# Kernel optimization log

Hardware: AMD Instinct MI355X
Metric: run time of the kernel (lower is better)

Reference implementation:

```python
import jax, jax.numpy as jnp
import numpy as np

N_NODES = 100000
N_EDGES = 1600000


def setup_inputs() -> dict:
    key = jax.random.key(0)
    ks = jax.random.split(key, 12)
    s = lambda d: 1.0 / np.sqrt(d)
    inp = {
        "x": jax.random.normal(ks[0], (N_NODES, 64), dtype=jnp.float32),
        "edge_index": jax.random.randint(ks[1], (2, N_EDGES), 0, N_NODES, dtype=jnp.int64),
        "W_embed": jax.random.normal(ks[2], (64, 128), dtype=jnp.float32) * s(64),
        "eps1": jnp.zeros((), jnp.float32),
        "w1a": jax.random.normal(ks[3], (128, 128), dtype=jnp.float32) * s(128),
        "b1a": jnp.zeros((128,), jnp.float32),
        "w1b": jax.random.normal(ks[4], (128, 128), dtype=jnp.float32) * s(128),
        "b1b": jnp.zeros((128,), jnp.float32),
        "eps2": jnp.zeros((), jnp.float32),
        "w2a": jax.random.normal(ks[5], (128, 256), dtype=jnp.float32) * s(128),
        "b2a": jnp.zeros((256,), jnp.float32),
        "w2b": jax.random.normal(ks[6], (256, 128), dtype=jnp.float32) * s(256),
        "b2b": jnp.zeros((128,), jnp.float32),
        "eps3": jnp.zeros((), jnp.float32),
        "w3a": jax.random.normal(ks[7], (128, 256), dtype=jnp.float32) * s(128),
        "b3a": jnp.zeros((256,), jnp.float32),
        "w3b": jax.random.normal(ks[8], (256, 128), dtype=jnp.float32) * s(256),
        "b3b": jnp.zeros((128,), jnp.float32),
    }
    return inp


def _aggregate(h, src, dst, n):
    # GINConv sum aggregation: out[i] = sum_{(j,i) in E} h[j]
    return jax.ops.segment_sum(h[src], dst, num_segments=n)


def reference(x, edge_index, W_embed, eps1, w1a, b1a, w1b, b1b,
              eps2, w2a, b2a, w2b, b2b, eps3, w3a, b3a, w3b, b3b):
    src, dst = edge_index[0], edge_index[1]
    n = x.shape[0]
    # node_attr_encoder: linear embedding (dropout p=0 -> identity)
    h = x @ W_embed  # [N, dim]
    # conv1: nn((1+eps)*h + sum_neighbors), nn = Lin->ReLU->Lin
    z = (1.0 + eps1) * h + _aggregate(h, src, dst, n)
    h = jax.nn.relu(z @ w1a + b1a) @ w1b + b1b
    # conv2/conv3: nn = Lin->ReLU->Lin->ReLU
    z = (1.0 + eps2) * h + _aggregate(h, src, dst, n)
    h = jax.nn.relu(jax.nn.relu(z @ w2a + b2a) @ w2b + b2b)
    z = (1.0 + eps3) * h + _aggregate(h, src, dst, n)
    h = jax.nn.relu(jax.nn.relu(z @ w3a + b3a) @ w3b + b3b)
    return h
```

## Files before the change

### kernel.cpp

```cpp
#include <hip/hip_runtime.h>
#include <hip/hip_bf16.h>
#include <stdint.h>


typedef __attribute__((ext_vector_type(8))) short short8;
typedef __attribute__((ext_vector_type(16))) float float16v;
typedef __attribute__((ext_vector_type(4))) unsigned int uint4v;

#define BKT 512
#define NBMAX 256

#define MFMA32 __builtin_amdgcn_mfma_f32_32x32x16_bf16

union U4S8 { uint4v u; short8 s; };

__device__ __forceinline__ float b2f_lo(unsigned int u) {
    return __uint_as_float(u << 16);
}
__device__ __forceinline__ float b2f_hi(unsigned int u) {
    return __uint_as_float(u & 0xffff0000u);
}
__device__ __forceinline__ unsigned short f2b(float f) {
    unsigned int u = __float_as_uint(f);
    return (unsigned short)((u + 0x7fffu + ((u >> 16) & 1u)) >> 16);
}
__device__ __forceinline__ unsigned cvtpk_bf16(float a, float b) {
    unsigned r;
    asm("v_cvt_pk_bf16_f32 %0, %1, %2" : "=v"(r) : "v"(a), "v"(b));
    return r;
}
__device__ __forceinline__ void perm32swap(unsigned& a, unsigned& b) {
    asm("v_permlane32_swap_b32 %0, %1" : "+v"(a), "+v"(b));
}

__global__ void detect_i64_kernel(const unsigned int* ei, int* flag) {
    if (threadIdx.x == 0) {
        int is64 = 1;
        for (int e = 0; e < 64; ++e)
            if (ei[2 * e + 1] != 0u) { is64 = 0; break; }
        *flag = is64;
    }
}

__device__ __forceinline__ int edge_at(const int* ei32, int is64, long long pos) {
    if (is64) return (int)(((const long long*)ei32)[pos]);
    return ei32[pos];
}

__global__ __launch_bounds__(256) void part_hist_kernel(
        const int* __restrict__ ei, const int* __restrict__ flag,
        int* __restrict__ bh, int E, int NB, int PB) {
    __shared__ int h[NBMAX];
    const int g = blockIdx.x, tid = threadIdx.x;
    const int is64 = *flag;
    for (int i = tid; i < NB; i += 256) h[i] = 0;
    __syncthreads();
    const int e0 = g * PB, e1 = min(e0 + PB, E);
    for (int e = e0 + tid; e < e1; e += 256) {
        int d = edge_at(ei, is64, (long long)E + e);
        atomicAdd(&h[d >> 9], 1);
    }
    __syncthreads();
    for (int i = tid; i < NB; i += 256) bh[i * gridDim.x + g] = h[i];
}

__global__ __launch_bounds__(1024) void scan1_kernel(
        const int* __restrict__ in, int* __restrict__ out,
        int* __restrict__ partial, int n) {
    __shared__ int sm[1024];
    const int t = threadIdx.x;
    const int i = blockIdx.x * 1024 + t;
    int v = (i < n) ? in[i] : 0;
    sm[t] = v;
    __syncthreads();
#pragma unroll
    for (int off = 1; off < 1024; off <<= 1) {
        int x = (t >= off) ? sm[t - off] : 0;
        __syncthreads();
        sm[t] += x;
        __syncthreads();
    }
    if (i < n) out[i] = sm[t] - v;
    if (t == 1023) partial[blockIdx.x] = sm[1023];
}

__global__ __launch_bounds__(256) void scan2_kernel(
        int* __restrict__ partial, int* __restrict__ blockoff, int g1) {
    __shared__ int sm[256];
    const int t = threadIdx.x;
    int v = (t < g1) ? partial[t] : 0;
    sm[t] = v;
    __syncthreads();
#pragma unroll
    for (int off = 1; off < 256; off <<= 1) {
        int x = (t >= off) ? sm[t - off] : 0;
        __syncthreads();
        sm[t] += x;
        __syncthreads();
    }
    blockoff[t] = sm[t] - v;
}

__global__ __launch_bounds__(1024) void scan3g_kernel(
        int* __restrict__ a, const int* __restrict__ blockoff, int n) {
    int i = blockIdx.x * 1024 + threadIdx.x;
    if (i < n) a[i] += blockoff[blockIdx.x];
}

__global__ __launch_bounds__(256) void part_scatter_kernel(
        const int* __restrict__ ei, const int* __restrict__ flag,
        const int* __restrict__ bhs, unsigned int* __restrict__ staged,
        int E, int NB, int PB) {
    __shared__ int cur[NBMAX];
    const int g = blockIdx.x, tid = threadIdx.x;
    const int is64 = *flag;
    for (int i = tid; i < NB; i += 256) cur[i] = bhs[i * gridDim.x + g];
    __syncthreads();
    const int e0 = g * PB, e1 = min(e0 + PB, E);
    for (int e = e0 + tid; e < e1; e += 256) {
        int d = edge_at(ei, is64, (long long)E + e);
        int s = edge_at(ei, is64, (long long)e);
        int b = d >> 9;
        int p = atomicAdd(&cur[b], 1);
        staged[p] = ((unsigned int)(d & (BKT - 1)) << 17) | (unsigned int)s;
    }
}

__global__ __launch_bounds__(256) void csr_local_kernel(
        const unsigned int* __restrict__ staged, const int* __restrict__ bhs,
        int* __restrict__ offs, int* __restrict__ csr, int N, int E, int NB, int G2) {
    __shared__ int hist[BKT];
    __shared__ int cur[BKT];
    const int b = blockIdx.x;
    const int tid = threadIdx.x;
    const int start = bhs[b * G2];
    const int end = (b + 1 < NB) ? bhs[(b + 1) * G2] : E;
    const int node0 = b * BKT;
    for (int i = tid; i < BKT; i += 256) hist[i] = 0;
    __syncthreads();
    for (int i = start + tid; i < end; i += 256)
        atomicAdd(&hist[staged[i] >> 17], 1);
    __syncthreads();
    const int i0 = tid * 2, i1 = i0 + 1;
    for (int off = 1; off < BKT; off <<= 1) {
        int v0 = (i0 >= off) ? hist[i0 - off] : 0;
        int v1 = (i1 >= off) ? hist[i1 - off] : 0;
        __syncthreads();
        hist[i0] += v0;
        hist[i1] += v1;
        __syncthreads();
    }
    for (int i = tid; i < BKT; i += 256) {
        int node = node0 + i;
        if (node < N) {
            int e0 = start + ((i == 0) ? 0 : hist[i - 1]);
            offs[node] = e0;
            cur[i] = e0;
        }
    }
    if (b == NB - 1 && tid == 0) offs[N] = E;
    __syncthreads();
    for (int i = start + tid; i < end; i += 256) {
        unsigned int v = staged[i];
        int dl = v >> 17;
        int src = (int)(v & 0x1ffff);
        int p = atomicAdd(&cur[dl], 1);
        csr[p] = src;
    }
}

struct PW { const float* W; unsigned short* o; int K; int KOUT; };
struct PWAll { PW d[7]; int cum[8]; };

__global__ __launch_bounds__(256) void packall_kernel(PWAll P) {
    int id = blockIdx.x * blockDim.x + threadIdx.x;
    if (id >= P.cum[7]) return;
    int w = 0;
#pragma unroll
    for (int k = 1; k < 7; ++k) w += (id >= P.cum[k]);
    const int local = id - P.cum[w];
    const float* W = P.d[w].W;
    unsigned short* out = P.d[w].o;
    const int K = P.d[w].K, KOUT = P.d[w].KOUT;
    const int KS = K / 16;
    const int l = local & 63;
    const int s = (local >> 6) % KS;
    const int T = local / (KS * 64);
    const int kbase = s * 16 + ((l >> 5) << 3);
    const int n = T * 32 + (l & 31);
#pragma unroll
    for (int j = 0; j < 8; ++j)
        out[(long long)local * 8 + j] = f2b(W[(long long)(kbase + j) * KOUT + n]);
}

__global__ __launch_bounds__(256) void mm_embed(
        const float* __restrict__ X, const unsigned short* __restrict__ Wp,
        unsigned short* __restrict__ out, int Mreal) {
    constexpr int KS = 4;
    const int tid = threadIdx.x;
    const int w = tid >> 6;
    const int l = tid & 63;
    const int lm = l & 31;
    const int lk = l >> 5;
    const int wr = w & 1, wc = w >> 1;
    const long long R0 = (long long)blockIdx.x * 128 + wr * 64;
    const int T0 = (wc * 64) >> 5;

    const long long r0 = (R0 + lm < Mreal) ? (R0 + lm) : (Mreal - 1);
    const long long r1 = (R0 + 32 + lm < Mreal) ? (R0 + 32 + lm) : (Mreal - 1);
    const float* xr0 = X + r0 * 64 + lk * 8;
    const float* xr1 = X + r1 * 64 + lk * 8;
    const unsigned short* bb0 = Wp + ((long long)T0 * KS * 64 + l) * 8;
    const unsigned short* bb1 = Wp + ((long long)(T0 + 1) * KS * 64 + l) * 8;

    float16v acc00 = {}, acc01 = {}, acc10 = {}, acc11 = {};
#pragma unroll
    for (int s = 0; s < KS; ++s) {
        float4 f0a = *(const float4*)(xr0 + s * 16);
        float4 f0b = *(const float4*)(xr0 + s * 16 + 4);
        float4 f1a = *(const float4*)(xr1 + s * 16);
        float4 f1b = *(const float4*)(xr1 + s * 16 + 4);
        short8 a0, a1;
        a0[0] = (short)f2b(f0a.x); a0[1] = (short)f2b(f0a.y);
        a0[2] = (short)f2b(f0a.z); a0[3] = (short)f2b(f0a.w);
        a0[4] = (short)f2b(f0b.x); a0[5] = (short)f2b(f0b.y);
        a0[6] = (short)f2b(f0b.z); a0[7] = (short)f2b(f0b.w);
        a1[0] = (short)f2b(f1a.x); a1[1] = (short)f2b(f1a.y);
        a1[2] = (short)f2b(f1a.z); a1[3] = (short)f2b(f1a.w);
        a1[4] = (short)f2b(f1b.x); a1[5] = (short)f2b(f1b.y);
        a1[6] = (short)f2b(f1b.z); a1[7] = (short)f2b(f1b.w);
        short8 b0 = *(const short8*)(bb0 + (long long)s * 64 * 8);
        short8 b1 = *(const short8*)(bb1 + (long long)s * 64 * 8);
        acc00 = MFMA32(a0, b0, acc00, 0, 0, 0);
        acc01 = MFMA32(a0, b1, acc01, 0, 0, 0);
        acc10 = MFMA32(a1, b0, acc10, 0, 0, 0);
        acc11 = MFMA32(a1, b1, acc11, 0, 0, 0);
    }
    auto st = [&](float16v acc, long long rb, int col) {
#pragma unroll
        for (int r = 0; r < 16; ++r) {
            long long row = rb + (r & 3) + 8 * (r >> 2);
            out[row * 128 + col] = f2b(acc[r]);
        }
    };
    const long long rbase = R0 + 4 * lk;
    st(acc00, rbase,      wc * 64 + lm);
    st(acc01, rbase,      wc * 64 + 32 + lm);
    st(acc10, rbase + 32, wc * 64 + lm);
    st(acc11, rbase + 32, wc * 64 + 32 + lm);
}

__global__ __launch_bounds__(256) void aggz_kernel(
        const unsigned short* __restrict__ H, const int* __restrict__ offs,
        const int* __restrict__ csr, const float* __restrict__ eps,
        unsigned short* __restrict__ Z, int n) {
    const int node = blockIdx.x * 16 + (threadIdx.x >> 4);
    const int c8 = (threadIdx.x & 15) << 3;
    if (node >= n) return;
    const int beg = offs[node];
    const int end = offs[node + 1];
    float a0 = 0.f, a1 = 0.f, a2 = 0.f, a3 = 0.f;
    float a4 = 0.f, a5 = 0.f, a6 = 0.f, a7 = 0.f;
    int i = beg;
    for (; i + 3 < end; i += 4) {
        const int j0 = csr[i], j1 = csr[i + 1], j2 = csr[i + 2], j3 = csr[i + 3];
        const uint4 u0 = *(const uint4*)(H + ((long long)j0 << 7) + c8);
        const uint4 u1 = *(const uint4*)(H + ((long long)j1 << 7) + c8);
        const uint4 u2 = *(const uint4*)(H + ((long long)j2 << 7) + c8);
        const uint4 u3 = *(const uint4*)(H + ((long long)j3 << 7) + c8);
        a0 += (b2f_lo(u0.x) + b2f_lo(u1.x)) + (b2f_lo(u2.x) + b2f_lo(u3.x));
        a1 += (b2f_hi(u0.x) + b2f_hi(u1.x)) + (b2f_hi(u2.x) + b2f_hi(u3.x));
        a2 += (b2f_lo(u0.y) + b2f_lo(u1.y)) + (b2f_lo(u2.y) + b2f_lo(u3.y));
        a3 += (b2f_hi(u0.y) + b2f_hi(u1.y)) + (b2f_hi(u2.y) + b2f_hi(u3.y));
        a4 += (b2f_lo(u0.z) + b2f_lo(u1.z)) + (b2f_lo(u2.z) + b2f_lo(u3.z));
        a5 += (b2f_hi(u0.z) + b2f_hi(u1.z)) + (b2f_hi(u2.z) + b2f_hi(u3.z));
        a6 += (b2f_lo(u0.w) + b2f_lo(u1.w)) + (b2f_lo(u2.w) + b2f_lo(u3.w));
        a7 += (b2f_hi(u0.w) + b2f_hi(u1.w)) + (b2f_hi(u2.w) + b2f_hi(u3.w));
    }
    for (; i < end; ++i) {
        const uint4 u0 = *(const uint4*)(H + ((long long)csr[i] << 7) + c8);
        a0 += b2f_lo(u0.x); a1 += b2f_hi(u0.x);
        a2 += b2f_lo(u0.y); a3 += b2f_hi(u0.y);
        a4 += b2f_lo(u0.z); a5 += b2f_hi(u0.z);
        a6 += b2f_lo(u0.w); a7 += b2f_hi(u0.w);
    }
    const uint4 uh = *(const uint4*)(H + ((long long)node << 7) + c8);
    const float e = 1.0f + eps[0];
    a0 = fmaf(e, b2f_lo(uh.x), a0); a1 = fmaf(e, b2f_hi(uh.x), a1);
    a2 = fmaf(e, b2f_lo(uh.y), a2); a3 = fmaf(e, b2f_hi(uh.y), a3);
    a4 = fmaf(e, b2f_lo(uh.z), a4); a5 = fmaf(e, b2f_hi(uh.z), a5);
    a6 = fmaf(e, b2f_lo(uh.w), a6); a7 = fmaf(e, b2f_hi(uh.w), a7);
    uint4 o;
    o.x = ((unsigned int)f2b(a1) << 16) | (unsigned int)f2b(a0);
    o.y = ((unsigned int)f2b(a3) << 16) | (unsigned int)f2b(a2);
    o.z = ((unsigned int)f2b(a5) << 16) | (unsigned int)f2b(a4);
    o.w = ((unsigned int)f2b(a7) << 16) | (unsigned int)f2b(a6);
    *(uint4*)(Z + ((long long)node << 7) + c8) = o;
}


#define CVT_TO_PA2(ACC, P0, P1) do {                                   \
        unsigned X1 = cvtpk_bf16((ACC)[0], (ACC)[1]);                  \
        unsigned Y1 = cvtpk_bf16((ACC)[4], (ACC)[5]);                  \
        unsigned X2 = cvtpk_bf16((ACC)[2], (ACC)[3]);                  \
        unsigned Y2 = cvtpk_bf16((ACC)[6], (ACC)[7]);                  \
        perm32swap(X1, Y1); perm32swap(X2, Y2);                        \
        U4S8 u0; u0.u[0] = X1; u0.u[1] = X2; u0.u[2] = Y1; u0.u[3] = Y2; \
        (P0) = u0.s;                                                   \
        unsigned X3 = cvtpk_bf16((ACC)[8], (ACC)[9]);                  \
        unsigned Y3 = cvtpk_bf16((ACC)[12], (ACC)[13]);                \
        unsigned X4 = cvtpk_bf16((ACC)[10], (ACC)[11]);                \
        unsigned Y4 = cvtpk_bf16((ACC)[14], (ACC)[15]);                \
        perm32swap(X3, Y3); perm32swap(X4, Y4);                        \
        U4S8 u1; u1.u[0] = X3; u1.u[1] = X4; u1.u[2] = Y3; u1.u[3] = Y4; \
        (P1) = u1.s;                                                   \
    } while (0)

template<int KMID, bool RELU2, bool OUTF32>
__global__ __launch_bounds__(512, 2) void fused_mlp3(
        const unsigned short* __restrict__ Zin,
        const unsigned short* __restrict__ Wap, const float* __restrict__ ba,
        const unsigned short* __restrict__ Wbp, const float* __restrict__ bb,
        void* __restrict__ outp, int Mreal, int nstrips) {
    constexpr int NF = KMID / 32;
    constexpr int NCH = KMID / 16;
    constexpr int WAS = 128 * KMID;
    __shared__ unsigned short wlds[KMID * 256];
    __shared__ float blds[KMID + 128];
    const int tid = threadIdx.x;

    {
        const uint4* sa = (const uint4*)Wap;
        const uint4* sb = (const uint4*)Wbp;
        uint4* da = (uint4*)wlds;
        uint4* db = (uint4*)(wlds + WAS);
#pragma unroll
        for (int i = tid; i < KMID * 16; i += 512) { da[i] = sa[i]; db[i] = sb[i]; }
        for (int i = tid; i < KMID; i += 512) blds[i] = ba[i];
        if (tid < 128) blds[KMID + tid] = bb[tid];
    }
    __syncthreads();

    const int wid = tid >> 6;
    const int l = tid & 63;
    const int lo = l & 31;
    const int hi = l >> 5;
    const int stride = gridDim.x * 8;
    int strip = blockIdx.x * 8 + wid;
    if (strip >= nstrips) return;

    auto zload = [&](int s_, short8* zz) {
        long long zr = (long long)s_ * 32 + lo;
        if (zr >= Mreal) zr = Mreal - 1;
        const unsigned short* zrow = Zin + zr * 128 + hi * 8;
#pragma unroll
        for (int s = 0; s < 8; ++s) zz[s] = *(const short8*)(zrow + s * 16);
    };

    short8 zc[8];
    zload(strip, zc);

    while (strip < nstrips) {
        const int nxt = strip + stride;
        float16v acc2[4] = {};
        short8 zn[8];

#pragma unroll
        for (int fp = 0; fp < NF / 2; ++fp) {
            if (fp == NF / 2 - 1) {
                if (nxt < nstrips) zload(nxt, zn);
            }
            const int f0 = 2 * fp, f1 = f0 + 1;
            float16v accA, accB;
#pragma unroll
            for (int q = 0; q < 4; ++q) {
                const float4 tA = *(const float4*)(blds + f0 * 32 + q * 8 + hi * 4);
                const float4 tB = *(const float4*)(blds + f1 * 32 + q * 8 + hi * 4);
                accA[4 * q + 0] = tA.x; accA[4 * q + 1] = tA.y;
                accA[4 * q + 2] = tA.z; accA[4 * q + 3] = tA.w;
                accB[4 * q + 0] = tB.x; accB[4 * q + 1] = tB.y;
                accB[4 * q + 2] = tB.z; accB[4 * q + 3] = tB.w;
            }
            const unsigned short* wa0 = wlds + ((long long)(f0 * 8) * 64 + l) * 8;
            const unsigned short* wa1 = wlds + ((long long)(f1 * 8) * 64 + l) * 8;
#pragma unroll
            for (int s = 0; s < 8; ++s) {
                short8 a0 = *(const short8*)(wa0 + s * 64 * 8);
                short8 a1 = *(const short8*)(wa1 + s * 64 * 8);
                accA = MFMA32(a0, zc[s], accA, 0, 0, 0);
                accB = MFMA32(a1, zc[s], accB, 0, 0, 0);
            }
#pragma unroll
            for (int r = 0; r < 16; ++r) {
                accA[r] = fmaxf(accA[r], 0.f);
                accB[r] = fmaxf(accB[r], 0.f);
            }
            short8 pa0, pa1, pa2, pa3;
            CVT_TO_PA2(accA, pa0, pa1);
            CVT_TO_PA2(accB, pa2, pa3);
            const unsigned short* wb = wlds + WAS + ((long long)(fp * 4) * 64 + l) * 8;
#pragma unroll
            for (int g = 0; g < 4; ++g) {
                const unsigned short* wbg = wb + (long long)g * NCH * 64 * 8;
                short8 b0 = *(const short8*)(wbg);
                short8 b1 = *(const short8*)(wbg + 64 * 8);
                short8 b2 = *(const short8*)(wbg + 2 * 64 * 8);
                short8 b3 = *(const short8*)(wbg + 3 * 64 * 8);
                acc2[g] = MFMA32(pa0, b0, acc2[g], 0, 0, 0);
                acc2[g] = MFMA32(pa1, b1, acc2[g], 0, 0, 0);
                acc2[g] = MFMA32(pa2, b2, acc2[g], 0, 0, 0);
                acc2[g] = MFMA32(pa3, b3, acc2[g], 0, 0, 0);
            }
        }

#pragma unroll
        for (int g = 0; g < 4; ++g) {
            const int col = g * 32 + lo;
            const float bv = blds[KMID + col];
#pragma unroll
            for (int r = 0; r < 16; ++r) {
                float v = acc2[g][r] + bv;
                if (RELU2) v = fmaxf(v, 0.f);
                const long long node = (long long)strip * 32 + (r & 3) + 8 * (r >> 2) + 4 * hi;
                if (node < Mreal) {
                    if (OUTF32) ((float*)outp)[node * 128 + col] = v;
                    else ((unsigned short*)outp)[node * 128 + col] = f2b(v);
                }
            }
        }

        strip = nxt;
        if (strip < nstrips) {
#pragma unroll
            for (int s = 0; s < 8; ++s) zc[s] = zn[s];
        }
    }
}

extern "C" void kernel_launch(void* const* d_in, const int* in_sizes, int n_in,
                              void* d_out, int out_size, void* d_ws, size_t ws_size,
                              hipStream_t stream) {
    const float* x    = (const float*)d_in[0];
    const int*   ei   = (const int*)d_in[1];
    const float* Wemb = (const float*)d_in[2];
    const float* eps1 = (const float*)d_in[3];
    const float* w1a  = (const float*)d_in[4];
    const float* b1a  = (const float*)d_in[5];
    const float* w1b  = (const float*)d_in[6];
    const float* b1b  = (const float*)d_in[7];
    const float* eps2 = (const float*)d_in[8];
    const float* w2a  = (const float*)d_in[9];
    const float* b2a  = (const float*)d_in[10];
    const float* w2b  = (const float*)d_in[11];
    const float* b2b  = (const float*)d_in[12];
    const float* eps3 = (const float*)d_in[13];
    const float* w3a  = (const float*)d_in[14];
    const float* b3a  = (const float*)d_in[15];
    const float* w3b  = (const float*)d_in[16];
    const float* b3b  = (const float*)d_in[17];

    const int N = in_sizes[0] / 64;
    const int E = in_sizes[1] / 2;
    const int Mpad = ((N + 127) / 128) * 128;
    const int NB = (N + BKT - 1) / BKT;
    const int G2 = 1024;
    const int PB = (E + G2 - 1) / G2;
    const int BH = NB * G2;

    char* ws = (char*)d_ws;
    size_t off = 0;
    auto alloc = [&](size_t bytes) -> void* {
        void* p = ws + off;
        off = (off + bytes + 255) & ~(size_t)255;
        return p;
    };
    unsigned short* Ha  = (unsigned short*)alloc((size_t)Mpad * 128 * 2);
    unsigned short* Hb2 = (unsigned short*)alloc((size_t)Mpad * 128 * 2);
    unsigned short* Zb  = (unsigned short*)alloc((size_t)Mpad * 128 * 2);
    unsigned short* pWe = (unsigned short*)alloc((size_t)64 * 128 * 2);
    unsigned short* p1a = (unsigned short*)alloc((size_t)128 * 128 * 2);
    unsigned short* p1b = (unsigned short*)alloc((size_t)128 * 128 * 2);
    unsigned short* p2a = (unsigned short*)alloc((size_t)128 * 256 * 2);
    unsigned short* p2b = (unsigned short*)alloc((size_t)256 * 128 * 2);
    unsigned short* p3a = (unsigned short*)alloc((size_t)128 * 256 * 2);
    unsigned short* p3b = (unsigned short*)alloc((size_t)256 * 128 * 2);
    int* offs = (int*)alloc((size_t)(N + 1) * 4);
    int* csr  = (int*)alloc((size_t)E * 4);
    unsigned int* staged = (unsigned int*)alloc((size_t)E * 4);
    int* bh   = (int*)alloc((size_t)BH * 4);
    int* bhs  = (int*)alloc((size_t)BH * 4);
    int* part = (int*)alloc(1024);
    int* boff = (int*)alloc(1024);
    int* flag = (int*)alloc(256);

    detect_i64_kernel<<<1, 64, 0, stream>>>((const unsigned int*)ei, flag);
    part_hist_kernel<<<G2, 256, 0, stream>>>(ei, flag, bh, E, NB, PB);
    const int G1 = (BH + 1023) / 1024;
    scan1_kernel<<<G1, 1024, 0, stream>>>(bh, bhs, part, BH);
    scan2_kernel<<<1, 256, 0, stream>>>(part, boff, G1);
    scan3g_kernel<<<G1, 1024, 0, stream>>>(bhs, boff, BH);
    part_scatter_kernel<<<G2, 256, 0, stream>>>(ei, flag, bhs, staged, E, NB, PB);
    csr_local_kernel<<<NB, 256, 0, stream>>>(staged, bhs, offs, csr, N, E, NB, G2);

    {
        PWAll P;
        const PW descs[7] = {
            {Wemb, pWe, 64, 128}, {w1a, p1a, 128, 128}, {w1b, p1b, 128, 128},
            {w2a, p2a, 128, 256}, {w2b, p2b, 256, 128}, {w3a, p3a, 128, 256},
            {w3b, p3b, 256, 128}};
        int c = 0;
        for (int k = 0; k < 7; ++k) {
            P.d[k] = descs[k];
            P.cum[k] = c;
            c += (descs[k].KOUT / 32) * (descs[k].K / 16) * 64;
        }
        P.cum[7] = c;
        packall_kernel<<<(c + 255) / 256, 256, 0, stream>>>(P);
    }

    const int MMB = Mpad / 128;
    const int AGB = (N + 15) / 16;
    const int NSTRIP = (N + 31) / 32;
    const int MLPG = 256;

    mm_embed<<<MMB, 256, 0, stream>>>(x, pWe, Ha, N);

    aggz_kernel<<<AGB, 256, 0, stream>>>(Ha, offs, csr, eps1, Zb, N);
    fused_mlp3<128, false, false><<<MLPG, 512, 0, stream>>>(Zb, p1a, b1a, p1b, b1b, Hb2, N, NSTRIP);

    aggz_kernel<<<AGB, 256, 0, stream>>>(Hb2, offs, csr, eps2, Zb, N);
    fused_mlp3<256, true, false><<<MLPG, 512, 0, stream>>>(Zb, p2a, b2a, p2b, b2b, Ha, N, NSTRIP);

    aggz_kernel<<<AGB, 256, 0, stream>>>(Ha, offs, csr, eps3, Zb, N);
    fused_mlp3<256, true, true><<<MLPG, 512, 0, stream>>>(Zb, p3a, b3a, p3b, b3b, d_out, N, NSTRIP);
}
```

Measured before the change: 435.4 us.

## Add 12-wave fused MLP kernel reading Z from global; inline int64 detection

Adds fused_mlp5, a 768-thread MLP kernel where each wave handles its own 32-node strip. It reads Z rows straight from global memory instead of the register-prefetched pipeline of fused_mlp3. The new kernel replaces layers 1 and 3, while layer 2 keeps the old kernel. The separate int64 detection kernel is removed, and each block of the partition kernels now detects the index width itself. The aim is more waves for latency hiding and one fewer launch, at the cost of redundant detection reads and less explicit prefetching.

```diff
diff --git a/kernel.cpp b/kernel.cpp
--- a/kernel.cpp
+++ b/kernel.cpp
@@ -33,28 +33,28 @@
     asm("v_permlane32_swap_b32 %0, %1" : "+v"(a), "+v"(b));
 }
 
-__global__ void detect_i64_kernel(const unsigned int* ei, int* flag) {
-    if (threadIdx.x == 0) {
-        int is64 = 1;
-        for (int e = 0; e < 64; ++e)
-            if (ei[2 * e + 1] != 0u) { is64 = 0; break; }
-        *flag = is64;
-    }
-}
-
 __device__ __forceinline__ int edge_at(const int* ei32, int is64, long long pos) {
     if (is64) return (int)(((const long long*)ei32)[pos]);
     return ei32[pos];
 }
 
+__device__ __forceinline__ int detect_is64(const int* ei) {
+    const unsigned int* eu = (const unsigned int*)ei;
+    int is64 = 1;
+    for (int e = 0; e < 64; ++e)
+        if (eu[2 * e + 1] != 0u) { is64 = 0; break; }
+    return is64;
+}
+
 __global__ __launch_bounds__(256) void part_hist_kernel(
-        const int* __restrict__ ei, const int* __restrict__ flag,
-        int* __restrict__ bh, int E, int NB, int PB) {
+        const int* __restrict__ ei, int* __restrict__ bh, int E, int NB, int PB) {
     __shared__ int h[NBMAX];
+    __shared__ int is64sh;
     const int g = blockIdx.x, tid = threadIdx.x;
-    const int is64 = *flag;
     for (int i = tid; i < NB; i += 256) h[i] = 0;
-    __syncthreads();
+    if (tid == 0) is64sh = detect_is64(ei);
+    __syncthreads();
+    const int is64 = is64sh;
     const int e0 = g * PB, e1 = min(e0 + PB, E);
     for (int e = e0 + tid; e < e1; e += 256) {
         int d = edge_at(ei, is64, (long long)E + e);
@@ -108,14 +108,15 @@
 }
 
 __global__ __launch_bounds__(256) void part_scatter_kernel(
-        const int* __restrict__ ei, const int* __restrict__ flag,
-        const int* __restrict__ bhs, unsigned int* __restrict__ staged,
-        int E, int NB, int PB) {
+        const int* __restrict__ ei, const int* __restrict__ bhs,
+        unsigned int* __restrict__ staged, int E, int NB, int PB) {
     __shared__ int cur[NBMAX];
+    __shared__ int is64sh;
     const int g = blockIdx.x, tid = threadIdx.x;
-    const int is64 = *flag;
     for (int i = tid; i < NB; i += 256) cur[i] = bhs[i * gridDim.x + g];
-    __syncthreads();
+    if (tid == 0) is64sh = detect_is64(ei);
+    __syncthreads();
+    const int is64 = is64sh;
     const int e0 = g * PB, e1 = min(e0 + PB, E);
     for (int e = e0 + tid; e < e1; e += 256) {
         int d = edge_at(ei, is64, (long long)E + e);
@@ -298,7 +299,6 @@
     *(uint4*)(Z + ((long long)node << 7) + c8) = o;
 }
 
-
 #define CVT_TO_PA2(ACC, P0, P1) do {                                   \
         unsigned X1 = cvtpk_bf16((ACC)[0], (ACC)[1]);                  \
         unsigned Y1 = cvtpk_bf16((ACC)[4], (ACC)[5]);                  \
@@ -433,6 +433,105 @@
         if (strip < nstrips) {
 #pragma unroll
             for (int s = 0; s < 8; ++s) zc[s] = zn[s];
+        }
+    }
+}
+
+template<int KMID, bool RELU2, bool OUTF32>
+__global__ __launch_bounds__(768, 3) void fused_mlp5(
+        const unsigned short* __restrict__ Zin,
+        const unsigned short* __restrict__ Wap, const float* __restrict__ ba,
+        const unsigned short* __restrict__ Wbp, const float* __restrict__ bb,
+        void* __restrict__ outp, int Mreal, int nstrips) {
+    constexpr int NF = KMID / 32;
+    constexpr int NCH = KMID / 16;
+    constexpr int WAS = 128 * KMID;
+    __shared__ unsigned short wlds[KMID * 256];
+    __shared__ float blds[KMID + 128];
+    const int tid = threadIdx.x;
+
+    {
+        const uint4* sa = (const uint4*)Wap;
+        const uint4* sb = (const uint4*)Wbp;
+        uint4* da = (uint4*)wlds;
+        uint4* db = (uint4*)(wlds + WAS);
+        for (int i = tid; i < KMID * 16; i += 768) { da[i] = sa[i]; db[i] = sb[i]; }
+        for (int i = tid; i < KMID; i += 768) blds[i] = ba[i];
+        if (tid < 128) blds[KMID + tid] = bb[tid];
+    }
+    __syncthreads();
+
+    const int wid = tid >> 6;
+    const int l = tid & 63;
+    const int lo = l & 31;
+    const int hi = l >> 5;
+    const int stride = gridDim.x * 12;
+
+    for (int strip = blockIdx.x * 12 + wid; strip < nstrips; strip += stride) {
+        const long long node0 = (long long)strip * 32;
+        long long zr = node0 + lo;
+        if (zr >= Mreal) zr = Mreal - 1;
+        const unsigned short* zrow = Zin + zr * 128 + hi * 8;
+
+        float16v acc2[4] = {};
+
+#pragma unroll 1
+        for (int f = 0; f < NF; ++f) {
+            float16v accA;
+#pragma unroll
+            for (int q = 0; q < 4; ++q) {
+                const float4 tA = *(const float4*)(blds + f * 32 + q * 8 + hi * 4);
+                accA[4 * q + 0] = tA.x; accA[4 * q + 1] = tA.y;
+                accA[4 * q + 2] = tA.z; accA[4 * q + 3] = tA.w;
+            }
+            const unsigned short* wa = wlds + (f * 8 * 64 + l) * 8;
+            {
+                short8 z0 = *(const short8*)(zrow + 0 * 16);
+                short8 z1 = *(const short8*)(zrow + 1 * 16);
+                short8 z2 = *(const short8*)(zrow + 2 * 16);
+                short8 z3 = *(const short8*)(zrow + 3 * 16);
+                accA = MFMA32(*(const short8*)(wa + 0 * 64 * 8), z0, accA, 0, 0, 0);
+                accA = MFMA32(*(const short8*)(wa + 1 * 64 * 8), z1, accA, 0, 0, 0);
+                accA = MFMA32(*(const short8*)(wa + 2 * 64 * 8), z2, accA, 0, 0, 0);
+                accA = MFMA32(*(const short8*)(wa + 3 * 64 * 8), z3, accA, 0, 0, 0);
+            }
+            {
+                short8 z4 = *(const short8*)(zrow + 4 * 16);
+                short8 z5 = *(const short8*)(zrow + 5 * 16);
+                short8 z6 = *(const short8*)(zrow + 6 * 16);
+                short8 z7 = *(const short8*)(zrow + 7 * 16);
+                accA = MFMA32(*(const short8*)(wa + 4 * 64 * 8), z4, accA, 0, 0, 0);
+                accA = MFMA32(*(const short8*)(wa + 5 * 64 * 8), z5, accA, 0, 0, 0);
+                accA = MFMA32(*(const short8*)(wa + 6 * 64 * 8), z6, accA, 0, 0, 0);
+                accA = MFMA32(*(const short8*)(wa + 7 * 64 * 8), z7, accA, 0, 0, 0);
+            }
+#pragma unroll
+            for (int r = 0; r < 16; ++r) accA[r] = fmaxf(accA[r], 0.f);
+            short8 pa0, pa1;
+            CVT_TO_PA2(accA, pa0, pa1);
+            const unsigned short* wb = wlds + WAS + ((2 * f) * 64 + l) * 8;
+#pragma unroll
+            for (int g = 0; g < 4; ++g) {
+                const unsigned short* wbg = wb + g * NCH * 64 * 8;
+                acc2[g] = MFMA32(pa0, *(const short8*)(wbg), acc2[g], 0, 0, 0);
+                acc2[g] = MFMA32(pa1, *(const short8*)(wbg + 64 * 8), acc2[g], 0, 0, 0);
+            }
+        }
+
+#pragma unroll
+        for (int g = 0; g < 4; ++g) {
+            const int col = g * 32 + lo;
+            const float bv = blds[KMID + col];
+#pragma unroll
+            for (int r = 0; r < 16; ++r) {
+                float v = acc2[g][r] + bv;
+                if (RELU2) v = fmaxf(v, 0.f);
+                const long long node = node0 + (r & 3) + 8 * (r >> 2) + 4 * hi;
+                if (node < Mreal) {
+                    if (OUTF32) ((float*)outp)[node * 128 + col] = v;
+                    else ((unsigned short*)outp)[node * 128 + col] = f2b(v);
+                }
+            }
         }
     }
 }
@@ -491,15 +590,13 @@
     int* bhs  = (int*)alloc((size_t)BH * 4);
     int* part = (int*)alloc(1024);
     int* boff = (int*)alloc(1024);
-    int* flag = (int*)alloc(256);
-
-    detect_i64_kernel<<<1, 64, 0, stream>>>((const unsigned int*)ei, flag);
-    part_hist_kernel<<<G2, 256, 0, stream>>>(ei, flag, bh, E, NB, PB);
+
+    part_hist_kernel<<<G2, 256, 0, stream>>>(ei, bh, E, NB, PB);
     const int G1 = (BH + 1023) / 1024;
     scan1_kernel<<<G1, 1024, 0, stream>>>(bh, bhs, part, BH);
     scan2_kernel<<<1, 256, 0, stream>>>(part, boff, G1);
     scan3g_kernel<<<G1, 1024, 0, stream>>>(bhs, boff, BH);
-    part_scatter_kernel<<<G2, 256, 0, stream>>>(ei, flag, bhs, staged, E, NB, PB);
+    part_scatter_kernel<<<G2, 256, 0, stream>>>(ei, bhs, staged, E, NB, PB);
     csr_local_kernel<<<NB, 256, 0, stream>>>(staged, bhs, offs, csr, N, E, NB, G2);
 
     {
@@ -526,11 +623,11 @@
     mm_embed<<<MMB, 256, 0, stream>>>(x, pWe, Ha, N);
 
     aggz_kernel<<<AGB, 256, 0, stream>>>(Ha, offs, csr, eps1, Zb, N);
-    fused_mlp3<128, false, false><<<MLPG, 512, 0, stream>>>(Zb, p1a, b1a, p1b, b1b, Hb2, N, NSTRIP);
+    fused_mlp5<128, false, false><<<MLPG, 768, 0, stream>>>(Zb, p1a, b1a, p1b, b1b, Hb2, N, NSTRIP);
 
     aggz_kernel<<<AGB, 256, 0, stream>>>(Hb2, offs, csr, eps2, Zb, N);
     fused_mlp3<256, true, false><<<MLPG, 512, 0, stream>>>(Zb, p2a, b2a, p2b, b2b, Ha, N, NSTRIP);
 
     aggz_kernel<<<AGB, 256, 0, stream>>>(Ha, offs, csr, eps3, Zb, N);
-    fused_mlp3<256, true, true><<<MLPG, 512, 0, stream>>>(Zb, p3a, b3a, p3b, b3b, d_out, N, NSTRIP);
-}
+    fused_mlp5<256, true, true><<<MLPG, 768, 0, stream>>>(Zb, p3a, b3a, p3b, b3b, d_out, N, NSTRIP);
+}
```

Result: no change. 436.0 us (+0.1%).

## Fuse neighbor aggregation into MLP kernel and fold int64 detection into partition kernels

Applied to the files above, without the earlier changes.

Each wave now gathers neighbor rows for its own 32-node strip, writes the aggregated Z rows to a global scratch buffer, and reads them back for the MFMA MLP. This removes three aggregation launches and lets gather latency overlap with MLP work in other waves. The standalone int64-detect kernel is also dropped; each partition block does the check itself. In exchange, the aggregation now runs on only 256 blocks of 512 threads with launch bounds tuned for the MLP, so it loses the wide parallelism of the old gather kernel, and the next-strip Z prefetch is gone.

```diff
diff --git a/kernel.cpp b/kernel.cpp
--- a/kernel.cpp
+++ b/kernel.cpp
@@ -33,28 +33,28 @@
     asm("v_permlane32_swap_b32 %0, %1" : "+v"(a), "+v"(b));
 }
 
-__global__ void detect_i64_kernel(const unsigned int* ei, int* flag) {
-    if (threadIdx.x == 0) {
-        int is64 = 1;
-        for (int e = 0; e < 64; ++e)
-            if (ei[2 * e + 1] != 0u) { is64 = 0; break; }
-        *flag = is64;
-    }
-}
-
 __device__ __forceinline__ int edge_at(const int* ei32, int is64, long long pos) {
     if (is64) return (int)(((const long long*)ei32)[pos]);
     return ei32[pos];
 }
 
+__device__ __forceinline__ int detect_is64(const int* ei) {
+    const unsigned int* eu = (const unsigned int*)ei;
+    int is64 = 1;
+    for (int e = 0; e < 64; ++e)
+        if (eu[2 * e + 1] != 0u) { is64 = 0; break; }
+    return is64;
+}
+
 __global__ __launch_bounds__(256) void part_hist_kernel(
-        const int* __restrict__ ei, const int* __restrict__ flag,
-        int* __restrict__ bh, int E, int NB, int PB) {
+        const int* __restrict__ ei, int* __restrict__ bh, int E, int NB, int PB) {
     __shared__ int h[NBMAX];
+    __shared__ int is64sh;
     const int g = blockIdx.x, tid = threadIdx.x;
-    const int is64 = *flag;
     for (int i = tid; i < NB; i += 256) h[i] = 0;
-    __syncthreads();
+    if (tid == 0) is64sh = detect_is64(ei);
+    __syncthreads();
+    const int is64 = is64sh;
     const int e0 = g * PB, e1 = min(e0 + PB, E);
     for (int e = e0 + tid; e < e1; e += 256) {
         int d = edge_at(ei, is64, (long long)E + e);
@@ -108,14 +108,15 @@
 }
 
 __global__ __launch_bounds__(256) void part_scatter_kernel(
-        const int* __restrict__ ei, const int* __restrict__ flag,
-        const int* __restrict__ bhs, unsigned int* __restrict__ staged,
-        int E, int NB, int PB) {
+        const int* __restrict__ ei, const int* __restrict__ bhs,
+        unsigned int* __restrict__ staged, int E, int NB, int PB) {
     __shared__ int cur[NBMAX];
+    __shared__ int is64sh;
     const int g = blockIdx.x, tid = threadIdx.x;
-    const int is64 = *flag;
     for (int i = tid; i < NB; i += 256) cur[i] = bhs[i * gridDim.x + g];
-    __syncthreads();
+    if (tid == 0) is64sh = detect_is64(ei);
+    __syncthreads();
+    const int is64 = is64sh;
     const int e0 = g * PB, e1 = min(e0 + PB, E);
     for (int e = e0 + tid; e < e1; e += 256) {
         int d = edge_at(ei, is64, (long long)E + e);
@@ -250,55 +251,6 @@
     st(acc11, rbase + 32, wc * 64 + 32 + lm);
 }
 
-__global__ __launch_bounds__(256) void aggz_kernel(
-        const unsigned short* __restrict__ H, const int* __restrict__ offs,
-        const int* __restrict__ csr, const float* __restrict__ eps,
-        unsigned short* __restrict__ Z, int n) {
-    const int node = blockIdx.x * 16 + (threadIdx.x >> 4);
-    const int c8 = (threadIdx.x & 15) << 3;
-    if (node >= n) return;
-    const int beg = offs[node];
-    const int end = offs[node + 1];
-    float a0 = 0.f, a1 = 0.f, a2 = 0.f, a3 = 0.f;
-    float a4 = 0.f, a5 = 0.f, a6 = 0.f, a7 = 0.f;
-    int i = beg;
-    for (; i + 3 < end; i += 4) {
-        const int j0 = csr[i], j1 = csr[i + 1], j2 = csr[i + 2], j3 = csr[i + 3];
-        const uint4 u0 = *(const uint4*)(H + ((long long)j0 << 7) + c8);
-        const uint4 u1 = *(const uint4*)(H + ((long long)j1 << 7) + c8);
-        const uint4 u2 = *(const uint4*)(H + ((long long)j2 << 7) + c8);
-        const uint4 u3 = *(const uint4*)(H + ((long long)j3 << 7) + c8);
-        a0 += (b2f_lo(u0.x) + b2f_lo(u1.x)) + (b2f_lo(u2.x) + b2f_lo(u3.x));
-        a1 += (b2f_hi(u0.x) + b2f_hi(u1.x)) + (b2f_hi(u2.x) + b2f_hi(u3.x));
-        a2 += (b2f_lo(u0.y) + b2f_lo(u1.y)) + (b2f_lo(u2.y) + b2f_lo(u3.y));
-        a3 += (b2f_hi(u0.y) + b2f_hi(u1.y)) + (b2f_hi(u2.y) + b2f_hi(u3.y));
-        a4 += (b2f_lo(u0.z) + b2f_lo(u1.z)) + (b2f_lo(u2.z) + b2f_lo(u3.z));
-        a5 += (b2f_hi(u0.z) + b2f_hi(u1.z)) + (b2f_hi(u2.z) + b2f_hi(u3.z));
-        a6 += (b2f_lo(u0.w) + b2f_lo(u1.w)) + (b2f_lo(u2.w) + b2f_lo(u3.w));
-        a7 += (b2f_hi(u0.w) + b2f_hi(u1.w)) + (b2f_hi(u2.w) + b2f_hi(u3.w));
-    }
-    for (; i < end; ++i) {
-        const uint4 u0 = *(const uint4*)(H + ((long long)csr[i] << 7) + c8);
-        a0 += b2f_lo(u0.x); a1 += b2f_hi(u0.x);
-        a2 += b2f_lo(u0.y); a3 += b2f_hi(u0.y);
-        a4 += b2f_lo(u0.z); a5 += b2f_hi(u0.z);
-        a6 += b2f_lo(u0.w); a7 += b2f_hi(u0.w);
-    }
-    const uint4 uh = *(const uint4*)(H + ((long long)node << 7) + c8);
-    const float e = 1.0f + eps[0];
-    a0 = fmaf(e, b2f_lo(uh.x), a0); a1 = fmaf(e, b2f_hi(uh.x), a1);
-    a2 = fmaf(e, b2f_lo(uh.y), a2); a3 = fmaf(e, b2f_hi(uh.y), a3);
-    a4 = fmaf(e, b2f_lo(uh.z), a4); a5 = fmaf(e, b2f_hi(uh.z), a5);
-    a6 = fmaf(e, b2f_lo(uh.w), a6); a7 = fmaf(e, b2f_hi(uh.w), a7);
-    uint4 o;
-    o.x = ((unsigned int)f2b(a1) << 16) | (unsigned int)f2b(a0);
-    o.y = ((unsigned int)f2b(a3) << 16) | (unsigned int)f2b(a2);
-    o.z = ((unsigned int)f2b(a5) << 16) | (unsigned int)f2b(a4);
-    o.w = ((unsigned int)f2b(a7) << 16) | (unsigned int)f2b(a6);
-    *(uint4*)(Z + ((long long)node << 7) + c8) = o;
-}
-
-
 #define CVT_TO_PA2(ACC, P0, P1) do {                                   \
         unsigned X1 = cvtpk_bf16((ACC)[0], (ACC)[1]);                  \
         unsigned Y1 = cvtpk_bf16((ACC)[4], (ACC)[5]);                  \
@@ -317,8 +269,11 @@
     } while (0)
 
 template<int KMID, bool RELU2, bool OUTF32>
-__global__ __launch_bounds__(512, 2) void fused_mlp3(
-        const unsigned short* __restrict__ Zin,
+__global__ __launch_bounds__(512, 2) void fused_aggmlp(
+        const unsigned short* __restrict__ H,
+        const int* __restrict__ offs, const int* __restrict__ csr,
+        const float* __restrict__ epsp,
+        unsigned short* __restrict__ Zb,
         const unsigned short* __restrict__ Wap, const float* __restrict__ ba,
         const unsigned short* __restrict__ Wbp, const float* __restrict__ bb,
         void* __restrict__ outp, int Mreal, int nstrips) {
@@ -345,31 +300,71 @@
     const int l = tid & 63;
     const int lo = l & 31;
     const int hi = l >> 5;
+    const int c8 = (l & 15) << 3;
+    const float e = 1.0f + epsp[0];
     const int stride = gridDim.x * 8;
-    int strip = blockIdx.x * 8 + wid;
-    if (strip >= nstrips) return;
-
-    auto zload = [&](int s_, short8* zz) {
-        long long zr = (long long)s_ * 32 + lo;
+
+    for (int strip = blockIdx.x * 8 + wid; strip < nstrips; strip += stride) {
+        const long long node0 = (long long)strip * 32;
+
+        const unsigned short* Hc = H + c8;
+#pragma unroll 1
+        for (int rnd = 0; rnd < 8; ++rnd) {
+            const int node = (int)node0 + rnd * 4 + (l >> 4);
+            if (node < Mreal) {
+                const int beg = offs[node];
+                const int end = offs[node + 1];
+                float a0 = 0.f, a1 = 0.f, a2 = 0.f, a3 = 0.f;
+                float a4 = 0.f, a5 = 0.f, a6 = 0.f, a7 = 0.f;
+                int i = beg;
+                for (; i + 3 < end; i += 4) {
+                    const int j0 = csr[i], j1 = csr[i + 1], j2 = csr[i + 2], j3 = csr[i + 3];
+                    const uint4 u0 = *(const uint4*)(Hc + ((long long)j0 << 7));
+                    const uint4 u1 = *(const uint4*)(Hc + ((long long)j1 << 7));
+                    const uint4 u2 = *(const uint4*)(Hc + ((long long)j2 << 7));
+                    const uint4 u3 = *(const uint4*)(Hc + ((long long)j3 << 7));
+                    a0 += (b2f_lo(u0.x) + b2f_lo(u1.x)) + (b2f_lo(u2.x) + b2f_lo(u3.x));
+                    a1 += (b2f_hi(u0.x) + b2f_hi(u1.x)) + (b2f_hi(u2.x) + b2f_hi(u3.x));
+                    a2 += (b2f_lo(u0.y) + b2f_lo(u1.y)) + (b2f_lo(u2.y) + b2f_lo(u3.y));
+                    a3 += (b2f_hi(u0.y) + b2f_hi(u1.y)) + (b2f_hi(u2.y) + b2f_hi(u3.y));
+                    a4 += (b2f_lo(u0.z) + b2f_lo(u1.z)) + (b2f_lo(u2.z) + b2f_lo(u3.z));
+                    a5 += (b2f_hi(u0.z) + b2f_hi(u1.z)) + (b2f_hi(u2.z) + b2f_hi(u3.z));
+                    a6 += (b2f_lo(u0.w) + b2f_lo(u1.w)) + (b2f_lo(u2.w) + b2f_lo(u3.w));
+                    a7 += (b2f_hi(u0.w) + b2f_hi(u1.w)) + (b2f_hi(u2.w) + b2f_hi(u3.w));
+                }
+                for (; i < end; ++i) {
+                    const uint4 u0 = *(const uint4*)(Hc + ((long long)csr[i] << 7));
+                    a0 += b2f_lo(u0.x); a1 += b2f_hi(u0.x);
+                    a2 += b2f_lo(u0.y); a3 += b2f_hi(u0.y);
+                    a4 += b2f_lo(u0.z); a5 += b2f_hi(u0.z);
+                    a6 += b2f_lo(u0.w); a7 += b2f_hi(u0.w);
+                }
+                const uint4 uh = *(const uint4*)(Hc + ((long long)node << 7));
+                a0 = fmaf(e, b2f_lo(uh.x), a0); a1 = fmaf(e, b2f_hi(uh.x), a1);
+                a2 = fmaf(e, b2f_lo(uh.y), a2); a3 = fmaf(e, b2f_hi(uh.y), a3);
+                a4 = fmaf(e, b2f_lo(uh.z), a4); a5 = fmaf(e, b2f_hi(uh.z), a5);
+                a6 = fmaf(e, b2f_lo(uh.w), a6); a7 = fmaf(e, b2f_hi(uh.w), a7);
+                uint4 o;
+                o.x = ((unsigned int)f2b(a1) << 16) | (unsigned int)f2b(a0);
+                o.y = ((unsigned int)f2b(a3) << 16) | (unsigned int)f2b(a2);
+                o.z = ((unsigned int)f2b(a5) << 16) | (unsigned int)f2b(a4);
+                o.w = ((unsigned int)f2b(a7) << 16) | (unsigned int)f2b(a6);
+                *(uint4*)(Zb + ((long long)node << 7) + c8) = o;
+            }
+        }
+        asm volatile("s_waitcnt vmcnt(0)" ::: "memory");
+
+        long long zr = node0 + lo;
         if (zr >= Mreal) zr = Mreal - 1;
-        const unsigned short* zrow = Zin + zr * 128 + hi * 8;
-#pragma unroll
-        for (int s = 0; s < 8; ++s) zz[s] = *(const short8*)(zrow + s * 16);
-    };
-
-    short8 zc[8];
-    zload(strip, zc);
-
-    while (strip < nstrips) {
-        const int nxt = strip + stride;
+        const unsigned short* zrow = Zb + zr * 128 + hi * 8;
+        short8 zc[8];
+#pragma unroll
+        for (int s = 0; s < 8; ++s) zc[s] = *(const short8*)(zrow + s * 16);
+
         float16v acc2[4] = {};
-        short8 zn[8];
 
 #pragma unroll
         for (int fp = 0; fp < NF / 2; ++fp) {
-            if (fp == NF / 2 - 1) {
-                if (nxt < nstrips) zload(nxt, zn);
-            }
             const int f0 = 2 * fp, f1 = f0 + 1;
             float16v accA, accB;
 #pragma unroll
@@ -421,18 +416,12 @@
             for (int r = 0; r < 16; ++r) {
                 float v = acc2[g][r] + bv;
                 if (RELU2) v = fmaxf(v, 0.f);
-                const long long node = (long long)strip * 32 + (r & 3) + 8 * (r >> 2) + 4 * hi;
+                const long long node = node0 + (r & 3) + 8 * (r >> 2) + 4 * hi;
                 if (node < Mreal) {
                     if (OUTF32) ((float*)outp)[node * 128 + col] = v;
                     else ((unsigned short*)outp)[node * 128 + col] = f2b(v);
                 }
             }
-        }
-
-        strip = nxt;
-        if (strip < nstrips) {
-#pragma unroll
-            for (int s = 0; s < 8; ++s) zc[s] = zn[s];
         }
     }
 }
@@ -491,15 +480,13 @@
     int* bhs  = (int*)alloc((size_t)BH * 4);
     int* part = (int*)alloc(1024);
     int* boff = (int*)alloc(1024);
-    int* flag = (int*)alloc(256);
-
-    detect_i64_kernel<<<1, 64, 0, stream>>>((const unsigned int*)ei, flag);
-    part_hist_kernel<<<G2, 256, 0, stream>>>(ei, flag, bh, E, NB, PB);
+
+    part_hist_kernel<<<G2, 256, 0, stream>>>(ei, bh, E, NB, PB);
     const int G1 = (BH + 1023) / 1024;
     scan1_kernel<<<G1, 1024, 0, stream>>>(bh, bhs, part, BH);
     scan2_kernel<<<1, 256, 0, stream>>>(part, boff, G1);
     scan3g_kernel<<<G1, 1024, 0, stream>>>(bhs, boff, BH);
-    part_scatter_kernel<<<G2, 256, 0, stream>>>(ei, flag, bhs, staged, E, NB, PB);
+    part_scatter_kernel<<<G2, 256, 0, stream>>>(ei, bhs, staged, E, NB, PB);
     csr_local_kernel<<<NB, 256, 0, stream>>>(staged, bhs, offs, csr, N, E, NB, G2);
 
     {
@@ -519,18 +506,17 @@
     }
 
     const int MMB = Mpad / 128;
-    const int AGB = (N + 15) / 16;
     const int NSTRIP = (N + 31) / 32;
     const int MLPG = 256;
 
     mm_embed<<<MMB, 256, 0, stream>>>(x, pWe, Ha, N);
 
-    aggz_kernel<<<AGB, 256, 0, stream>>>(Ha, offs, csr, eps1, Zb, N);
-    fused_mlp3<128, false, false><<<MLPG, 512, 0, stream>>>(Zb, p1a, b1a, p1b, b1b, Hb2, N, NSTRIP);
-
-    aggz_kernel<<<AGB, 256, 0, stream>>>(Hb2, offs, csr, eps2, Zb, N);
-    fused_mlp3<256, true, false><<<MLPG, 512, 0, stream>>>(Zb, p2a, b2a, p2b, b2b, Ha, N, NSTRIP);
-
-    aggz_kernel<<<AGB, 256, 0, stream>>>(Ha, offs, csr, eps3, Zb, N);
-    fused_mlp3<256, true, true><<<MLPG, 512, 0, stream>>>(Zb, p3a, b3a, p3b, b3b, d_out, N, NSTRIP);
-}
+    fused_aggmlp<128, false, false><<<MLPG, 512, 0, stream>>>(
+        Ha, offs, csr, eps1, Zb, p1a, b1a, p1b, b1b, Hb2, N, NSTRIP);
+
+    fused_aggmlp<256, true, false><<<MLPG, 512, 0, stream>>>(
+        Hb2, offs, csr, eps2, Zb, p2a, b2a, p2b, b2b, Ha, N, NSTRIP);
+
+    fused_aggmlp<256, true, true><<<MLPG, 512, 0, stream>>>(
+        Ha, offs, csr, eps3, Zb, p3a, b3a, p3b, b3b, d_out, N, NSTRIP);
+}
```

After: 584.5 us. +34.3%, slower.

## Use atomic work-stealing for MLP strips and fold i64 detection into partition kernels

Applied to the files above, without the earlier changes.

The fused MLP kernels now hand out 32-row strips through a global atomic counter per layer instead of a fixed grid stride, so waves that finish early pick up more work. The counters are zeroed inside the embedding kernel. The separate int64-detect launch is removed and each partition block now repeats the detection itself. The conv2 MLP grid also drops to 128 blocks. This trades one kernel launch and static imbalance for an atomic per strip per wave, redundant detection reads in every block, and a dependence on mm_embed running before the MLPs to reset the counters.

```diff
diff --git a/kernel.cpp b/kernel.cpp
--- a/kernel.cpp
+++ b/kernel.cpp
@@ -33,28 +33,28 @@
     asm("v_permlane32_swap_b32 %0, %1" : "+v"(a), "+v"(b));
 }
 
-__global__ void detect_i64_kernel(const unsigned int* ei, int* flag) {
-    if (threadIdx.x == 0) {
-        int is64 = 1;
-        for (int e = 0; e < 64; ++e)
-            if (ei[2 * e + 1] != 0u) { is64 = 0; break; }
-        *flag = is64;
-    }
-}
-
 __device__ __forceinline__ int edge_at(const int* ei32, int is64, long long pos) {
     if (is64) return (int)(((const long long*)ei32)[pos]);
     return ei32[pos];
 }
 
+__device__ __forceinline__ int detect_is64(const int* ei) {
+    const unsigned int* eu = (const unsigned int*)ei;
+    int is64 = 1;
+    for (int e = 0; e < 64; ++e)
+        if (eu[2 * e + 1] != 0u) { is64 = 0; break; }
+    return is64;
+}
+
 __global__ __launch_bounds__(256) void part_hist_kernel(
-        const int* __restrict__ ei, const int* __restrict__ flag,
-        int* __restrict__ bh, int E, int NB, int PB) {
+        const int* __restrict__ ei, int* __restrict__ bh, int E, int NB, int PB) {
     __shared__ int h[NBMAX];
+    __shared__ int is64sh;
     const int g = blockIdx.x, tid = threadIdx.x;
-    const int is64 = *flag;
     for (int i = tid; i < NB; i += 256) h[i] = 0;
-    __syncthreads();
+    if (tid == 0) is64sh = detect_is64(ei);
+    __syncthreads();
+    const int is64 = is64sh;
     const int e0 = g * PB, e1 = min(e0 + PB, E);
     for (int e = e0 + tid; e < e1; e += 256) {
         int d = edge_at(ei, is64, (long long)E + e);
@@ -108,14 +108,15 @@
 }
 
 __global__ __launch_bounds__(256) void part_scatter_kernel(
-        const int* __restrict__ ei, const int* __restrict__ flag,
-        const int* __restrict__ bhs, unsigned int* __restrict__ staged,
-        int E, int NB, int PB) {
+        const int* __restrict__ ei, const int* __restrict__ bhs,
+        unsigned int* __restrict__ staged, int E, int NB, int PB) {
     __shared__ int cur[NBMAX];
+    __shared__ int is64sh;
     const int g = blockIdx.x, tid = threadIdx.x;
-    const int is64 = *flag;
     for (int i = tid; i < NB; i += 256) cur[i] = bhs[i * gridDim.x + g];
-    __syncthreads();
+    if (tid == 0) is64sh = detect_is64(ei);
+    __syncthreads();
+    const int is64 = is64sh;
     const int e0 = g * PB, e1 = min(e0 + PB, E);
     for (int e = e0 + tid; e < e1; e += 256) {
         int d = edge_at(ei, is64, (long long)E + e);
@@ -195,9 +196,10 @@
 
 __global__ __launch_bounds__(256) void mm_embed(
         const float* __restrict__ X, const unsigned short* __restrict__ Wp,
-        unsigned short* __restrict__ out, int Mreal) {
+        unsigned short* __restrict__ out, int Mreal, int* __restrict__ ctrs) {
     constexpr int KS = 4;
     const int tid = threadIdx.x;
+    if (blockIdx.x == 0 && tid < 3) ctrs[tid] = 0;
     const int w = tid >> 6;
     const int l = tid & 63;
     const int lm = l & 31;
@@ -298,7 +300,6 @@
     *(uint4*)(Z + ((long long)node << 7) + c8) = o;
 }
 
-
 #define CVT_TO_PA2(ACC, P0, P1) do {                                   \
         unsigned X1 = cvtpk_bf16((ACC)[0], (ACC)[1]);                  \
         unsigned Y1 = cvtpk_bf16((ACC)[4], (ACC)[5]);                  \
@@ -317,11 +318,11 @@
     } while (0)
 
 template<int KMID, bool RELU2, bool OUTF32>
-__global__ __launch_bounds__(512, 2) void fused_mlp3(
+__global__ __launch_bounds__(512, 2) void fused_mlp6(
         const unsigned short* __restrict__ Zin,
         const unsigned short* __restrict__ Wap, const float* __restrict__ ba,
         const unsigned short* __restrict__ Wbp, const float* __restrict__ bb,
-        void* __restrict__ outp, int Mreal, int nstrips) {
+        void* __restrict__ outp, int Mreal, int nstrips, int* __restrict__ ctr) {
     constexpr int NF = KMID / 32;
     constexpr int NCH = KMID / 16;
     constexpr int WAS = 128 * KMID;
@@ -341,13 +342,15 @@
     }
     __syncthreads();
 
-    const int wid = tid >> 6;
     const int l = tid & 63;
     const int lo = l & 31;
     const int hi = l >> 5;
-    const int stride = gridDim.x * 8;
-    int strip = blockIdx.x * 8 + wid;
-    if (strip >= nstrips) return;
+
+    auto steal = [&]() -> int {
+        int s = 0;
+        if (l == 0) s = atomicAdd(ctr, 1);
+        return __shfl(s, 0);
+    };
 
     auto zload = [&](int s_, short8* zz) {
         long long zr = (long long)s_ * 32 + lo;
@@ -357,11 +360,13 @@
         for (int s = 0; s < 8; ++s) zz[s] = *(const short8*)(zrow + s * 16);
     };
 
+    int strip = steal();
+    if (strip >= nstrips) return;
     short8 zc[8];
     zload(strip, zc);
 
-    while (strip < nstrips) {
-        const int nxt = strip + stride;
+    while (true) {
+        const int nxt = steal();
         float16v acc2[4] = {};
         short8 zn[8];
 
@@ -429,11 +434,10 @@
             }
         }
 
+        if (nxt >= nstrips) break;
         strip = nxt;
-        if (strip < nstrips) {
-#pragma unroll
-            for (int s = 0; s < 8; ++s) zc[s] = zn[s];
-        }
+#pragma unroll
+        for (int s = 0; s < 8; ++s) zc[s] = zn[s];
     }
 }
 
@@ -491,15 +495,14 @@
     int* bhs  = (int*)alloc((size_t)BH * 4);
     int* part = (int*)alloc(1024);
     int* boff = (int*)alloc(1024);
-    int* flag = (int*)alloc(256);
-
-    detect_i64_kernel<<<1, 64, 0, stream>>>((const unsigned int*)ei, flag);
-    part_hist_kernel<<<G2, 256, 0, stream>>>(ei, flag, bh, E, NB, PB);
+    int* mctr = (int*)alloc(256);
+
+    part_hist_kernel<<<G2, 256, 0, stream>>>(ei, bh, E, NB, PB);
     const int G1 = (BH + 1023) / 1024;
     scan1_kernel<<<G1, 1024, 0, stream>>>(bh, bhs, part, BH);
     scan2_kernel<<<1, 256, 0, stream>>>(part, boff, G1);
     scan3g_kernel<<<G1, 1024, 0, stream>>>(bhs, boff, BH);
-    part_scatter_kernel<<<G2, 256, 0, stream>>>(ei, flag, bhs, staged, E, NB, PB);
+    part_scatter_kernel<<<G2, 256, 0, stream>>>(ei, bhs, staged, E, NB, PB);
     csr_local_kernel<<<NB, 256, 0, stream>>>(staged, bhs, offs, csr, N, E, NB, G2);
 
     {
@@ -521,16 +524,18 @@
     const int MMB = Mpad / 128;
     const int AGB = (N + 15) / 16;
     const int NSTRIP = (N + 31) / 32;
-    const int MLPG = 256;
-
-    mm_embed<<<MMB, 256, 0, stream>>>(x, pWe, Ha, N);
+
+    mm_embed<<<MMB, 256, 0, stream>>>(x, pWe, Ha, N, mctr);
 
     aggz_kernel<<<AGB, 256, 0, stream>>>(Ha, offs, csr, eps1, Zb, N);
-    fused_mlp3<128, false, false><<<MLPG, 512, 0, stream>>>(Zb, p1a, b1a, p1b, b1b, Hb2, N, NSTRIP);
+    fused_mlp6<128, false, false><<<256, 512, 0, stream>>>(
+        Zb, p1a, b1a, p1b, b1b, Hb2, N, NSTRIP, mctr + 0);
 
     aggz_kernel<<<AGB, 256, 0, stream>>>(Hb2, offs, csr, eps2, Zb, N);
-    fused_mlp3<256, true, false><<<MLPG, 512, 0, stream>>>(Zb, p2a, b2a, p2b, b2b, Ha, N, NSTRIP);
+    fused_mlp6<256, true, false><<<128, 512, 0, stream>>>(
+        Zb, p2a, b2a, p2b, b2b, Ha, N, NSTRIP, mctr + 1);
 
     aggz_kernel<<<AGB, 256, 0, stream>>>(Ha, offs, csr, eps3, Zb, N);
-    fused_mlp3<256, true, true><<<MLPG, 512, 0, stream>>>(Zb, p3a, b3a, p3b, b3b, d_out, N, NSTRIP);
-}
+    fused_mlp6<256, true, true><<<256, 512, 0, stream>>>(
+        Zb, p3a, b3a, p3b, b3b, d_out, N, NSTRIP, mctr + 2);
+}
```

New measurement: 574.9 us. 32.0% more time.
